# Optimization experiments

Measured on AMD Instinct MI355X. Metric: run time of the kernel, lower is better.

The kernel has to match this reference:

```python
import jax, jax.numpy as jnp
import numpy as np

K = 3        # prediction_steps
SKIP = 1     # skip_step (forward default)
NEG = 64     # opt.negative_samples
EPS = 1e-11  # ExpNLLLoss epsilon


def setup_inputs() -> dict:
    key = jax.random.key(0)
    ks = jax.random.split(key, 8)
    B, C, H, W = 64, 256, 14, 14
    z = jax.random.normal(ks[0], (B, C, H, W), jnp.float32)
    c = jax.random.normal(ks[1], (B, C, H, W), jnp.float32)
    Wk = jax.random.normal(ks[2], (K, C, C), jnp.float32) / np.sqrt(C).astype(np.float32)
    inp = {"z": z, "c": c, "Wk": Wk}
    for k in range(1, K + 1):
        Hp = H - (k + SKIP)
        rows = Hp * W * B
        inp[f"neg_idx_k{k}"] = jax.random.randint(ks[2 + k], (rows * NEG,), 0, rows, dtype=jnp.int32)
    return inp


def _loss_k(z, c, Wk, neg_idx, k):
    # z, c: [B,C,H,W]; Wk: [Co,Ci] (1x1 conv); neg_idx: [(H-k-SKIP)*W*B*NEG]
    B, C, H, W = z.shape
    Hp = H - (k + SKIP)
    zt = z[:, :, k + SKIP:, :]                            # [B,Ci,Hp,W]
    ztwk = jnp.einsum('oc,bchw->hwbo', Wk, zt)            # [Hp,W,B,Co] (1x1 conv + permute(2,3,0,1))
    flat = ztwk.reshape(Hp * W * B, -1)
    shuf = flat[neg_idx].reshape(Hp, W, B, NEG, -1)       # gathered negatives [Hp,W,B,N,Co]
    ctx = jnp.transpose(c[:, :, :Hp, :], (2, 3, 0, 1))    # context c[:,:,:-(k+SKIP),:] -> [Hp,W,B,Co]
    main = jnp.einsum('hwbc,hwbc->hwb', ctx, ztwk)[..., None]   # [Hp,W,B,1]
    negs = jnp.einsum('hwbc,hwbnc->hwbn', ctx, shuf)            # [Hp,W,B,N]
    log_fk = jnp.concatenate([main, negs], axis=-1)             # [Hp,W,B,1+N]
    log_fk = jnp.transpose(log_fk, (2, 3, 0, 1))                # [B,1+N,Hp,W]
    probs = jax.nn.softmax(log_fk, axis=1)
    # ExpNLLLoss, target class 0, reduction='mean'
    return -jnp.mean(jnp.log(probs[:, 0] + EPS))


def reference(z, c, Wk, neg_idx_k1, neg_idx_k2, neg_idx_k3):
    idxs = [neg_idx_k1, neg_idx_k2, neg_idx_k3]
    total = 0.0
    for k in range(1, K + 1):
        total = total + _loss_k(z, c, Wk[k - 1], idxs[k - 1], k)
    return total / K
```

## Files before the change

### kernel.cpp

```cpp
#include <hip/hip_runtime.h>
#include <math.h>


typedef short bf16x8 __attribute__((ext_vector_type(8)));
typedef float f32x4 __attribute__((ext_vector_type(4)));

static __device__ __forceinline__ unsigned short f2bf(float f) {
    union { float f; unsigned int u; } x; x.f = f;
    unsigned int r = x.u + 0x7fffu + ((x.u >> 16) & 1u);
    return (unsigned short)(r >> 16);
}

static __device__ __forceinline__ unsigned char f2e4m3(float f) {
    union { float f; unsigned int u; } x; x.f = f;
    unsigned int s = (x.u >> 24) & 0x80u;
    float af = fabsf(f);
    if (af > 448.f) af = 448.f;
    x.f = af;
    unsigned int u = x.u;
    int e = (int)(u >> 23) - 127;
    unsigned int out;
    if (af == 0.f) {
        out = 0u;
    } else if (e < -6) {
        int mq = (int)rintf(af * 512.f);
        out = (mq >= 8) ? 0x08u : (unsigned int)mq;
    } else {
        unsigned int r = u + 0x7FFFFu + ((u >> 20) & 1u);
        int e2 = (int)(r >> 23) - 127;
        if (e2 > 8) out = 0x7Eu;
        else out = (unsigned int)(((e2 + 7) << 3) | ((r >> 20) & 7u));
    }
    return (unsigned char)(s | out);
}

static __device__ __forceinline__ void gload_lds4(const void* g, void* l) {
    __builtin_amdgcn_global_load_lds(
        (const __attribute__((address_space(1))) void*)g,
        (__attribute__((address_space(3))) void*)l, 4, 0, 0);
}

__global__ void zero_out_kernel(float* out) { out[0] = 0.f; }

__global__ void cast_wk_kernel(const float* __restrict__ Wk, unsigned short* __restrict__ wkb) {
    int i = blockIdx.x * 256 + threadIdx.x;
    wkb[i] = f2bf(Wk[i]);
}

__global__ __launch_bounds__(256)
void transpose_z_kernel(const float* __restrict__ x, unsigned short* __restrict__ xt) {
    __shared__ float tile[16][201];
    const int tid = threadIdx.x;
    const int b  = blockIdx.x;
    const int c0 = blockIdx.y << 4;
    for (int i = tid; i < 16 * 196; i += 256) {
        int cc = i / 196;
        int hw = i - cc * 196;
        tile[cc][hw] = x[(size_t)((b << 8) + c0 + cc) * 196 + hw];
    }
    __syncthreads();
    for (int i = tid; i < 196 * 16; i += 256) {
        int hw = i >> 4;
        int cc = i & 15;
        xt[(size_t)((hw << 6) + b) * 256 + c0 + cc] = f2bf(tile[cc][hw]);
    }
}

__global__ __launch_bounds__(256)
void transpose_c8_kernel(const float* __restrict__ x, unsigned char* __restrict__ xt) {
    __shared__ float tile[16][201];
    const int tid = threadIdx.x;
    const int b  = blockIdx.x;
    const int c0 = blockIdx.y << 4;
    for (int i = tid; i < 16 * 196; i += 256) {
        int cc = i / 196;
        int hw = i - cc * 196;
        tile[cc][hw] = x[(size_t)((b << 8) + c0 + cc) * 196 + hw];
    }
    __syncthreads();
    for (int i = tid; i < 196 * 16; i += 256) {
        int hw = i >> 4;
        int cc = i & 15;
        xt[(size_t)((hw << 6) + b) * 256 + c0 + cc] = f2e4m3(tile[cc][hw]);
    }
}

#define PSTR 544
__global__ __launch_bounds__(256)
void proj_mfma_kernel(const unsigned short* __restrict__ zt,
                      const unsigned short* __restrict__ wkb,
                      unsigned char* __restrict__ ztwk) {
    __shared__ __align__(16) unsigned char smem[(64 + 32) * PSTR];
    unsigned char* smA = smem;
    unsigned char* smB = smem + 64 * PSTR;

    int x = blockIdx.x;
    int k, hw;
    if (x < 168)      { k = 0; hw = x; }
    else if (x < 322) { k = 1; hw = x - 168; }
    else              { k = 2; hw = x - 322; }
    const int o0 = blockIdx.y << 5;
    const int row0  = hw << 6;
    const int zrow0 = row0 + (((k + 2) * 14) << 6);
    unsigned char* zo = ztwk + (size_t)k * 10752 * 256;

    const int tid = threadIdx.x;
    const unsigned char* zsrc = (const unsigned char*)(zt + (size_t)zrow0 * 256);
    const unsigned char* bsrc = (const unsigned char*)(wkb + ((size_t)k << 16) + o0 * 256);

    #pragma unroll
    for (int i = 0; i < 8; ++i) {
        int sb = ((i << 8) + tid) << 4;
        int r = sb >> 9, off = sb & 511;
        *(int4*)(smA + r * PSTR + off) = *(const int4*)(zsrc + sb);
    }
    #pragma unroll
    for (int i = 0; i < 4; ++i) {
        int sb = ((i << 8) + tid) << 4;
        int r = sb >> 9, off = sb & 511;
        *(int4*)(smB + r * PSTR + off) = *(const int4*)(bsrc + sb);
    }
    __syncthreads();

    const int wv = tid >> 6, lane = tid & 63;
    const int m = lane & 15, kq = lane >> 4;
    f32x4 acc[2] = {};
    const unsigned short* aP  = (const unsigned short*)(smA + (size_t)((wv << 4) + m) * PSTR) + (kq << 3);
    const unsigned short* bP0 = (const unsigned short*)(smB + (size_t)m * PSTR) + (kq << 3);
    const unsigned short* bP1 = (const unsigned short*)(smB + (size_t)(16 + m) * PSTR) + (kq << 3);
    #pragma unroll
    for (int kk = 0; kk < 256; kk += 32) {
        bf16x8 af = *(const bf16x8*)(aP  + kk);
        bf16x8 b0 = *(const bf16x8*)(bP0 + kk);
        bf16x8 b1 = *(const bf16x8*)(bP1 + kk);
        acc[0] = __builtin_amdgcn_mfma_f32_16x16x32_bf16(af, b0, acc[0], 0, 0, 0);
        acc[1] = __builtin_amdgcn_mfma_f32_16x16x32_bf16(af, b1, acc[1], 0, 0, 0);
    }
    __syncthreads();
    unsigned char* cs = smA;
    #pragma unroll
    for (int nt = 0; nt < 2; ++nt)
        #pragma unroll
        for (int r = 0; r < 4; ++r)
            cs[(size_t)((wv << 4) + (kq << 2) + r) * 40 + (nt << 4) + m] =
                f2e4m3(acc[nt][r]);
    __syncthreads();
    {
        int r = tid >> 2, off = (tid & 3) << 3;
        unsigned long long v = *(const unsigned long long*)(cs + (size_t)r * 40 + off);
        *(unsigned long long*)(zo + (size_t)(row0 + r) * 256 + o0 + off) = v;
    }
}

#define ROWB 272
__global__ __launch_bounds__(128, 4)
void loss_mfma_kernel(const unsigned char* __restrict__ ct8,
                      const unsigned char* __restrict__ ztwk8,
                      const int* __restrict__ n0, const int* __restrict__ n1,
                      const int* __restrict__ n2, float* __restrict__ rowloss) {
    __shared__ __align__(16) unsigned char slab[65 * ROWB];
    __shared__ __align__(16) unsigned char ctx_s[256];
    __shared__ float sred[2][2];
    const int tid = threadIdx.x;
    const int wv = tid >> 6, lane = tid & 63;
    const int m = lane & 15, kq = lane >> 4;

    int x = blockIdx.x;
    int k; const int* nb_base;
    if (x < 10752)      { k = 0; nb_base = n0; }
    else if (x < 20608) { k = 1; nb_base = n1; x -= 10752; }
    else                { k = 2; nb_base = n2; x -= 20608; }
    const int row = x;
    const unsigned char* flat8 = ztwk8 + (size_t)k * 10752 * 256;
    const float wk = (k == 0) ? (1.f / (3.f * 10752.f))
                   : (k == 1) ? (1.f / (3.f * 9856.f))
                              : (1.f / (3.f * 8960.f));
    const int rbase = (k == 0) ? 0 : (k == 1) ? 10752 : 20608;

    const int myidx = nb_base[((size_t)row << 6) + lane];

    if (wv == 0) {
        gload_lds4(flat8 + (size_t)row * 256 + (lane << 2), slab);
        #pragma unroll
        for (int j = 1; j <= 32; ++j) {
            int idx = __builtin_amdgcn_readlane(myidx, j - 1);
            gload_lds4(flat8 + (size_t)idx * 256 + (lane << 2), slab + j * ROWB);
        }
    } else {
        gload_lds4(ct8 + (size_t)row * 256 + (lane << 2), ctx_s);
        #pragma unroll
        for (int j = 33; j <= 64; ++j) {
            int idx = __builtin_amdgcn_readlane(myidx, j - 1);
            gload_lds4(flat8 + (size_t)idx * 256 + (lane << 2), slab + j * ROWB);
        }
    }
    __syncthreads();

    f32x4 acc[3] = {};
    const int mt0 = (wv == 0) ? 0 : 3;
    int soff[3];
    #pragma unroll
    for (int t = 0; t < 3; ++t) {
        int slot = ((mt0 + t) << 4) + m;
        if (slot > 64) slot = 64;
        soff[t] = slot * ROWB + (kq << 3);
    }
    const unsigned char* cp = ctx_s + (kq << 3);
    #pragma unroll
    for (int kk = 0; kk < 8; ++kk) {
        long long bfrag = *(const long long*)(cp + (kk << 5));
        #pragma unroll
        for (int t = 0; t < 3; ++t) {
            if (t < 2 || wv == 0) {
                long long af = *(const long long*)(slab + soff[t] + (kk << 5));
                acc[t] = __builtin_amdgcn_mfma_f32_16x16x32_fp8_fp8(af, bfrag, acc[t], 0, 0, 0);
            }
        }
    }

    float m_l = -1e30f;
    if (wv == 0) {
        #pragma unroll
        for (int t = 0; t < 3; ++t)
            #pragma unroll
            for (int r = 0; r < 4; ++r) m_l = fmaxf(m_l, acc[t][r]);
    } else {
        #pragma unroll
        for (int r = 0; r < 4; ++r) m_l = fmaxf(m_l, acc[0][r]);
        if (kq == 0) m_l = fmaxf(m_l, acc[1][0]);
    }
    m_l = fmaxf(m_l, __shfl_xor(m_l, 16));
    m_l = fmaxf(m_l, __shfl_xor(m_l, 32));

    float s_l = 0.f;
    if (wv == 0) {
        #pragma unroll
        for (int t = 0; t < 3; ++t)
            #pragma unroll
            for (int r = 0; r < 4; ++r) s_l += __expf(acc[t][r] - m_l);
    } else {
        #pragma unroll
        for (int r = 0; r < 4; ++r) s_l += __expf(acc[0][r] - m_l);
        if (kq == 0) s_l += __expf(acc[1][0] - m_l);
    }
    s_l += __shfl_xor(s_l, 16);
    s_l += __shfl_xor(s_l, 32);

    float main_l = acc[0][0];
    if (lane == 0) { sred[wv][0] = m_l; sred[wv][1] = s_l; }
    __syncthreads();
    if (tid == 0) {
        float m0 = sred[0][0], s0 = sred[0][1];
        float m1 = sred[1][0], s1 = sred[1][1];
        float mg = fmaxf(m0, m1);
        float sg = s0 * __expf(m0 - mg) + s1 * __expf(m1 - mg);
        float p0 = __expf(main_l - mg) / sg;
        rowloss[rbase + row] = -logf(p0 + 1e-11f) * wk;
    }
}

__global__ __launch_bounds__(256)
void reduce_kernel(const float* __restrict__ rl, float* __restrict__ out) {
    float s = 0.f;
    const int stride = gridDim.x * blockDim.x;
    for (int i = blockIdx.x * blockDim.x + threadIdx.x; i < 29568; i += stride)
        s += rl[i];
    #pragma unroll
    for (int off = 32; off >= 1; off >>= 1) s += __shfl_xor(s, off);
    if ((threadIdx.x & 63) == 0) atomicAdd(out, s);
}

extern "C" void kernel_launch(void* const* d_in, const int* in_sizes, int n_in,
                              void* d_out, int out_size, void* d_ws, size_t ws_size,
                              hipStream_t stream) {
    const float* z  = (const float*)d_in[0];
    const float* c  = (const float*)d_in[1];
    const float* Wk = (const float*)d_in[2];
    const int* negs[3] = {(const int*)d_in[3], (const int*)d_in[4], (const int*)d_in[5]};
    float* out = (float*)d_out;

    char* p = (char*)d_ws;
    unsigned short* zt      = (unsigned short*)p;   p += (size_t)196 * 64 * 256 * 2;
    unsigned short* wkb     = (unsigned short*)p;   p += (size_t)3 * 65536 * 2;
    unsigned char*  ct8     = (unsigned char*)p;    p += (size_t)196 * 64 * 256;
    unsigned char*  ztwk8   = (unsigned char*)p;    p += (size_t)3 * 10752 * 256;
    float*          rowloss = (float*)p;

    zero_out_kernel<<<1, 1, 0, stream>>>(out);
    cast_wk_kernel<<<768, 256, 0, stream>>>(Wk, wkb);
    transpose_z_kernel<<<dim3(64, 16), 256, 0, stream>>>(z, zt);
    transpose_c8_kernel<<<dim3(64, 16), 256, 0, stream>>>(c, ct8);

    proj_mfma_kernel<<<dim3(462, 8), 256, 0, stream>>>(zt, wkb, ztwk8);

    loss_mfma_kernel<<<29568, 128, 0, stream>>>(ct8, ztwk8, negs[0], negs[1],
                                                negs[2], rowloss);
    reduce_kernel<<<32, 256, 0, stream>>>(rowloss, out);
}
```

Before: 161.4 us.

## Merge prep kernels and make loss kernel persistent with warp-specialized double buffering

Folds the Wk cast, output zeroing and both transposes into a single prep launch to cut launch overhead. The loss kernel now processes 16 rows per block, with one wave acting as a loader that fills the next row's gathered slab into a second LDS buffer while the other wave runs MFMAs and the softmax on the current buffer. This replaces 29568 tiny blocks with 1848 blocks and aims to overlap gather latency with compute. The cost is doubled LDS per block, lower occupancy (launch bounds 2), and only one wave doing the math.

```diff
diff --git a/kernel.cpp b/kernel.cpp
--- a/kernel.cpp
+++ b/kernel.cpp
@@ -40,48 +40,41 @@
         (__attribute__((address_space(3))) void*)l, 4, 0, 0);
 }
 
-__global__ void zero_out_kernel(float* out) { out[0] = 0.f; }
-
-__global__ void cast_wk_kernel(const float* __restrict__ Wk, unsigned short* __restrict__ wkb) {
-    int i = blockIdx.x * 256 + threadIdx.x;
-    wkb[i] = f2bf(Wk[i]);
-}
-
 __global__ __launch_bounds__(256)
-void transpose_z_kernel(const float* __restrict__ x, unsigned short* __restrict__ xt) {
+void prep_kernel(const float* __restrict__ z, const float* __restrict__ c,
+                 const float* __restrict__ Wk,
+                 unsigned short* __restrict__ zt, unsigned char* __restrict__ ct8,
+                 unsigned short* __restrict__ wkb, float* __restrict__ out) {
     __shared__ float tile[16][201];
     const int tid = threadIdx.x;
-    const int b  = blockIdx.x;
-    const int c0 = blockIdx.y << 4;
+    int x = blockIdx.x;
+    if (x < 768) {
+        int i = x * 256 + tid;
+        wkb[i] = f2bf(Wk[i]);
+        if (x == 0 && tid == 0) out[0] = 0.f;
+        return;
+    }
+    const bool isz = x < 1792;
+    const int local = isz ? (x - 768) : (x - 1792);
+    const float* src = isz ? z : c;
+    const int b  = local & 63;
+    const int c0 = (local >> 6) << 4;
     for (int i = tid; i < 16 * 196; i += 256) {
         int cc = i / 196;
         int hw = i - cc * 196;
-        tile[cc][hw] = x[(size_t)((b << 8) + c0 + cc) * 196 + hw];
-    }
-    __syncthreads();
-    for (int i = tid; i < 196 * 16; i += 256) {
-        int hw = i >> 4;
-        int cc = i & 15;
-        xt[(size_t)((hw << 6) + b) * 256 + c0 + cc] = f2bf(tile[cc][hw]);
-    }
-}
-
-__global__ __launch_bounds__(256)
-void transpose_c8_kernel(const float* __restrict__ x, unsigned char* __restrict__ xt) {
-    __shared__ float tile[16][201];
-    const int tid = threadIdx.x;
-    const int b  = blockIdx.x;
-    const int c0 = blockIdx.y << 4;
-    for (int i = tid; i < 16 * 196; i += 256) {
-        int cc = i / 196;
-        int hw = i - cc * 196;
-        tile[cc][hw] = x[(size_t)((b << 8) + c0 + cc) * 196 + hw];
-    }
-    __syncthreads();
-    for (int i = tid; i < 196 * 16; i += 256) {
-        int hw = i >> 4;
-        int cc = i & 15;
-        xt[(size_t)((hw << 6) + b) * 256 + c0 + cc] = f2e4m3(tile[cc][hw]);
+        tile[cc][hw] = src[(size_t)((b << 8) + c0 + cc) * 196 + hw];
+    }
+    __syncthreads();
+    if (isz) {
+        for (int i = tid; i < 196 * 16; i += 256) {
+            int hw = i >> 4, cc = i & 15;
+            zt[(size_t)((hw << 6) + b) * 256 + c0 + cc] = f2bf(tile[cc][hw]);
+        }
+    } else {
+        for (int i = tid; i < 196 * 16; i += 256) {
+            int hw = i >> 4, cc = i & 15;
+            ct8[(size_t)((hw << 6) + b) * 256 + c0 + cc] = f2e4m3(tile[cc][hw]);
+        }
     }
 }
 
@@ -153,109 +146,104 @@
 }
 
 #define ROWB 272
-__global__ __launch_bounds__(128, 4)
+#define TPB 16
+__global__ __launch_bounds__(128, 2)
 void loss_mfma_kernel(const unsigned char* __restrict__ ct8,
                       const unsigned char* __restrict__ ztwk8,
                       const int* __restrict__ n0, const int* __restrict__ n1,
                       const int* __restrict__ n2, float* __restrict__ rowloss) {
-    __shared__ __align__(16) unsigned char slab[65 * ROWB];
-    __shared__ __align__(16) unsigned char ctx_s[256];
-    __shared__ float sred[2][2];
+    __shared__ __align__(16) unsigned char slab[2][65 * ROWB];
+    __shared__ __align__(16) unsigned char ctx_s[2][256];
     const int tid = threadIdx.x;
     const int wv = tid >> 6, lane = tid & 63;
     const int m = lane & 15, kq = lane >> 4;
 
-    int x = blockIdx.x;
-    int k; const int* nb_base;
-    if (x < 10752)      { k = 0; nb_base = n0; }
-    else if (x < 20608) { k = 1; nb_base = n1; x -= 10752; }
-    else                { k = 2; nb_base = n2; x -= 20608; }
-    const int row = x;
+    const int task0 = blockIdx.x * TPB;
+    int k; const int* nb; int segbase;
+    if (task0 < 10752)      { k = 0; nb = n0; segbase = 0; }
+    else if (task0 < 20608) { k = 1; nb = n1; segbase = 10752; }
+    else                    { k = 2; nb = n2; segbase = 20608; }
+    const int row0 = task0 - segbase;
     const unsigned char* flat8 = ztwk8 + (size_t)k * 10752 * 256;
-    const float wk = (k == 0) ? (1.f / (3.f * 10752.f))
-                   : (k == 1) ? (1.f / (3.f * 9856.f))
-                              : (1.f / (3.f * 8960.f));
-    const int rbase = (k == 0) ? 0 : (k == 1) ? 10752 : 20608;
-
-    const int myidx = nb_base[((size_t)row << 6) + lane];
-
-    if (wv == 0) {
-        gload_lds4(flat8 + (size_t)row * 256 + (lane << 2), slab);
+    const float wkf = (k == 0) ? (1.f / (3.f * 10752.f))
+                    : (k == 1) ? (1.f / (3.f * 9856.f))
+                               : (1.f / (3.f * 8960.f));
+
+    int myidx_next = 0;
+    if (wv == 1) {
+        int idx0 = nb[((size_t)row0 << 6) + lane];
+        gload_lds4(flat8 + (size_t)row0 * 256 + (lane << 2), &slab[0][0]);
+        gload_lds4(ct8 + (size_t)row0 * 256 + (lane << 2), &ctx_s[0][0]);
         #pragma unroll
-        for (int j = 1; j <= 32; ++j) {
-            int idx = __builtin_amdgcn_readlane(myidx, j - 1);
-            gload_lds4(flat8 + (size_t)idx * 256 + (lane << 2), slab + j * ROWB);
-        }
-    } else {
-        gload_lds4(ct8 + (size_t)row * 256 + (lane << 2), ctx_s);
-        #pragma unroll
-        for (int j = 33; j <= 64; ++j) {
-            int idx = __builtin_amdgcn_readlane(myidx, j - 1);
-            gload_lds4(flat8 + (size_t)idx * 256 + (lane << 2), slab + j * ROWB);
-        }
-    }
-    __syncthreads();
-
-    f32x4 acc[3] = {};
-    const int mt0 = (wv == 0) ? 0 : 3;
-    int soff[3];
-    #pragma unroll
-    for (int t = 0; t < 3; ++t) {
-        int slot = ((mt0 + t) << 4) + m;
+        for (int j = 1; j <= 64; ++j) {
+            int idx = __builtin_amdgcn_readlane(idx0, j - 1);
+            gload_lds4(flat8 + (size_t)idx * 256 + (lane << 2), &slab[0][j * ROWB]);
+        }
+        myidx_next = nb[((size_t)(row0 + 1) << 6) + lane];
+    }
+    __syncthreads();
+
+    int soff[5];
+    #pragma unroll
+    for (int mt = 0; mt < 5; ++mt) {
+        int slot = (mt << 4) + m;
         if (slot > 64) slot = 64;
-        soff[t] = slot * ROWB + (kq << 3);
-    }
-    const unsigned char* cp = ctx_s + (kq << 3);
-    #pragma unroll
-    for (int kk = 0; kk < 8; ++kk) {
-        long long bfrag = *(const long long*)(cp + (kk << 5));
-        #pragma unroll
-        for (int t = 0; t < 3; ++t) {
-            if (t < 2 || wv == 0) {
-                long long af = *(const long long*)(slab + soff[t] + (kk << 5));
-                acc[t] = __builtin_amdgcn_mfma_f32_16x16x32_fp8_fp8(af, bfrag, acc[t], 0, 0, 0);
+        soff[mt] = slot * ROWB + (kq << 3);
+    }
+
+    for (int t = 0; t < TPB; ++t) {
+        const int buf = t & 1;
+        if (wv == 1) {
+            if (t + 1 < TPB) {
+                const int rn = row0 + t + 1;
+                const int nbuf = buf ^ 1;
+                gload_lds4(flat8 + (size_t)rn * 256 + (lane << 2), &slab[nbuf][0]);
+                gload_lds4(ct8 + (size_t)rn * 256 + (lane << 2), &ctx_s[nbuf][0]);
+                #pragma unroll
+                for (int j = 1; j <= 64; ++j) {
+                    int idx = __builtin_amdgcn_readlane(myidx_next, j - 1);
+                    gload_lds4(flat8 + (size_t)idx * 256 + (lane << 2),
+                               &slab[nbuf][j * ROWB]);
+                }
+                if (t + 2 < TPB)
+                    myidx_next = nb[((size_t)(row0 + t + 2) << 6) + lane];
             }
-        }
-    }
-
-    float m_l = -1e30f;
-    if (wv == 0) {
-        #pragma unroll
-        for (int t = 0; t < 3; ++t)
+        } else {
+            f32x4 acc[5] = {};
+            const unsigned char* sl = &slab[buf][0];
+            const unsigned char* cp = &ctx_s[buf][kq << 3];
             #pragma unroll
-            for (int r = 0; r < 4; ++r) m_l = fmaxf(m_l, acc[t][r]);
-    } else {
-        #pragma unroll
-        for (int r = 0; r < 4; ++r) m_l = fmaxf(m_l, acc[0][r]);
-        if (kq == 0) m_l = fmaxf(m_l, acc[1][0]);
-    }
-    m_l = fmaxf(m_l, __shfl_xor(m_l, 16));
-    m_l = fmaxf(m_l, __shfl_xor(m_l, 32));
-
-    float s_l = 0.f;
-    if (wv == 0) {
-        #pragma unroll
-        for (int t = 0; t < 3; ++t)
+            for (int kk = 0; kk < 8; ++kk) {
+                long long bfrag = *(const long long*)(cp + (kk << 5));
+                #pragma unroll
+                for (int mt = 0; mt < 5; ++mt) {
+                    long long af = *(const long long*)(sl + soff[mt] + (kk << 5));
+                    acc[mt] = __builtin_amdgcn_mfma_f32_16x16x32_fp8_fp8(
+                        af, bfrag, acc[mt], 0, 0, 0);
+                }
+            }
+            float m_l = -1e30f;
             #pragma unroll
-            for (int r = 0; r < 4; ++r) s_l += __expf(acc[t][r] - m_l);
-    } else {
-        #pragma unroll
-        for (int r = 0; r < 4; ++r) s_l += __expf(acc[0][r] - m_l);
-        if (kq == 0) s_l += __expf(acc[1][0] - m_l);
-    }
-    s_l += __shfl_xor(s_l, 16);
-    s_l += __shfl_xor(s_l, 32);
-
-    float main_l = acc[0][0];
-    if (lane == 0) { sred[wv][0] = m_l; sred[wv][1] = s_l; }
-    __syncthreads();
-    if (tid == 0) {
-        float m0 = sred[0][0], s0 = sred[0][1];
-        float m1 = sred[1][0], s1 = sred[1][1];
-        float mg = fmaxf(m0, m1);
-        float sg = s0 * __expf(m0 - mg) + s1 * __expf(m1 - mg);
-        float p0 = __expf(main_l - mg) / sg;
-        rowloss[rbase + row] = -logf(p0 + 1e-11f) * wk;
+            for (int mt = 0; mt < 4; ++mt)
+                #pragma unroll
+                for (int r = 0; r < 4; ++r) m_l = fmaxf(m_l, acc[mt][r]);
+            if (kq == 0) m_l = fmaxf(m_l, acc[4][0]);
+            m_l = fmaxf(m_l, __shfl_xor(m_l, 16));
+            m_l = fmaxf(m_l, __shfl_xor(m_l, 32));
+            float s_l = 0.f;
+            #pragma unroll
+            for (int mt = 0; mt < 4; ++mt)
+                #pragma unroll
+                for (int r = 0; r < 4; ++r) s_l += __expf(acc[mt][r] - m_l);
+            if (kq == 0) s_l += __expf(acc[4][0] - m_l);
+            s_l += __shfl_xor(s_l, 16);
+            s_l += __shfl_xor(s_l, 32);
+            if (lane == 0) {
+                float p0 = __expf(acc[0][0] - m_l) / s_l;
+                rowloss[segbase + row0 + t] = -logf(p0 + 1e-11f) * wkf;
+            }
+        }
+        __syncthreads();
     }
 }
 
@@ -286,14 +274,9 @@
     unsigned char*  ztwk8   = (unsigned char*)p;    p += (size_t)3 * 10752 * 256;
     float*          rowloss = (float*)p;
 
-    zero_out_kernel<<<1, 1, 0, stream>>>(out);
-    cast_wk_kernel<<<768, 256, 0, stream>>>(Wk, wkb);
-    transpose_z_kernel<<<dim3(64, 16), 256, 0, stream>>>(z, zt);
-    transpose_c8_kernel<<<dim3(64, 16), 256, 0, stream>>>(c, ct8);
-
+    prep_kernel<<<2816, 256, 0, stream>>>(z, c, Wk, zt, ct8, wkb, out);
     proj_mfma_kernel<<<dim3(462, 8), 256, 0, stream>>>(zt, wkb, ztwk8);
-
-    loss_mfma_kernel<<<29568, 128, 0, stream>>>(ct8, ztwk8, negs[0], negs[1],
-                                                negs[2], rowloss);
+    loss_mfma_kernel<<<1848, 128, 0, stream>>>(ct8, ztwk8, negs[0], negs[1],
+                                               negs[2], rowloss);
     reduce_kernel<<<32, 256, 0, stream>>>(rowloss, out);
 }
```

Result: slower. 167.8 us (+4.0%).

## Fuse prep kernels into one launch and reorder projection grid

Applied to the files above, without the earlier changes.

Merges the zero-init, Wk bf16 cast, z transpose and c fp8 transpose kernels into a single prep kernel that dispatches on block index, cutting three kernel launches and their gaps. The projection grid is swapped so the 8 output-column blocks for the same z rows are adjacent, which should improve L2 reuse of the z tile. The LDS row stride is also changed from 544 to 528, which alters bank-conflict behavior. The prep kernel adds a branch, but its blocks are independent.

```diff
diff --git a/kernel.cpp b/kernel.cpp
--- a/kernel.cpp
+++ b/kernel.cpp
@@ -40,52 +40,45 @@
         (__attribute__((address_space(3))) void*)l, 4, 0, 0);
 }
 
-__global__ void zero_out_kernel(float* out) { out[0] = 0.f; }
-
-__global__ void cast_wk_kernel(const float* __restrict__ Wk, unsigned short* __restrict__ wkb) {
-    int i = blockIdx.x * 256 + threadIdx.x;
-    wkb[i] = f2bf(Wk[i]);
-}
-
 __global__ __launch_bounds__(256)
-void transpose_z_kernel(const float* __restrict__ x, unsigned short* __restrict__ xt) {
+void prep_kernel(const float* __restrict__ z, const float* __restrict__ c,
+                 const float* __restrict__ Wk,
+                 unsigned short* __restrict__ zt, unsigned char* __restrict__ ct8,
+                 unsigned short* __restrict__ wkb, float* __restrict__ out) {
     __shared__ float tile[16][201];
     const int tid = threadIdx.x;
-    const int b  = blockIdx.x;
-    const int c0 = blockIdx.y << 4;
+    int x = blockIdx.x;
+    if (x < 768) {
+        int i = x * 256 + tid;
+        wkb[i] = f2bf(Wk[i]);
+        if (x == 0 && tid == 0) out[0] = 0.f;
+        return;
+    }
+    const bool isz = x < 1792;
+    const int local = isz ? (x - 768) : (x - 1792);
+    const float* src = isz ? z : c;
+    const int b  = local & 63;
+    const int c0 = (local >> 6) << 4;
     for (int i = tid; i < 16 * 196; i += 256) {
         int cc = i / 196;
         int hw = i - cc * 196;
-        tile[cc][hw] = x[(size_t)((b << 8) + c0 + cc) * 196 + hw];
-    }
-    __syncthreads();
-    for (int i = tid; i < 196 * 16; i += 256) {
-        int hw = i >> 4;
-        int cc = i & 15;
-        xt[(size_t)((hw << 6) + b) * 256 + c0 + cc] = f2bf(tile[cc][hw]);
-    }
-}
-
-__global__ __launch_bounds__(256)
-void transpose_c8_kernel(const float* __restrict__ x, unsigned char* __restrict__ xt) {
-    __shared__ float tile[16][201];
-    const int tid = threadIdx.x;
-    const int b  = blockIdx.x;
-    const int c0 = blockIdx.y << 4;
-    for (int i = tid; i < 16 * 196; i += 256) {
-        int cc = i / 196;
-        int hw = i - cc * 196;
-        tile[cc][hw] = x[(size_t)((b << 8) + c0 + cc) * 196 + hw];
-    }
-    __syncthreads();
-    for (int i = tid; i < 196 * 16; i += 256) {
-        int hw = i >> 4;
-        int cc = i & 15;
-        xt[(size_t)((hw << 6) + b) * 256 + c0 + cc] = f2e4m3(tile[cc][hw]);
-    }
-}
-
-#define PSTR 544
+        tile[cc][hw] = src[(size_t)((b << 8) + c0 + cc) * 196 + hw];
+    }
+    __syncthreads();
+    if (isz) {
+        for (int i = tid; i < 196 * 16; i += 256) {
+            int hw = i >> 4, cc = i & 15;
+            zt[(size_t)((hw << 6) + b) * 256 + c0 + cc] = f2bf(tile[cc][hw]);
+        }
+    } else {
+        for (int i = tid; i < 196 * 16; i += 256) {
+            int hw = i >> 4, cc = i & 15;
+            ct8[(size_t)((hw << 6) + b) * 256 + c0 + cc] = f2e4m3(tile[cc][hw]);
+        }
+    }
+}
+
+#define PSTR 528
 __global__ __launch_bounds__(256)
 void proj_mfma_kernel(const unsigned short* __restrict__ zt,
                       const unsigned short* __restrict__ wkb,
@@ -94,12 +87,12 @@
     unsigned char* smA = smem;
     unsigned char* smB = smem + 64 * PSTR;
 
-    int x = blockIdx.x;
+    int x = blockIdx.y;
     int k, hw;
     if (x < 168)      { k = 0; hw = x; }
     else if (x < 322) { k = 1; hw = x - 168; }
     else              { k = 2; hw = x - 322; }
-    const int o0 = blockIdx.y << 5;
+    const int o0 = blockIdx.x << 5;
     const int row0  = hw << 6;
     const int zrow0 = row0 + (((k + 2) * 14) << 6);
     unsigned char* zo = ztwk + (size_t)k * 10752 * 256;
@@ -286,13 +279,8 @@
     unsigned char*  ztwk8   = (unsigned char*)p;    p += (size_t)3 * 10752 * 256;
     float*          rowloss = (float*)p;
 
-    zero_out_kernel<<<1, 1, 0, stream>>>(out);
-    cast_wk_kernel<<<768, 256, 0, stream>>>(Wk, wkb);
-    transpose_z_kernel<<<dim3(64, 16), 256, 0, stream>>>(z, zt);
-    transpose_c8_kernel<<<dim3(64, 16), 256, 0, stream>>>(c, ct8);
-
-    proj_mfma_kernel<<<dim3(462, 8), 256, 0, stream>>>(zt, wkb, ztwk8);
-
+    prep_kernel<<<2816, 256, 0, stream>>>(z, c, Wk, zt, ct8, wkb, out);
+    proj_mfma_kernel<<<dim3(8, 462), 256, 0, stream>>>(zt, wkb, ztwk8);
     loss_mfma_kernel<<<29568, 128, 0, stream>>>(ct8, ztwk8, negs[0], negs[1],
                                                 negs[2], rowloss);
     reduce_kernel<<<32, 256, 0, stream>>>(rowloss, out);
```

After: 155.2 us. 3.9% less time.
